# Kernel optimization log

Hardware: AMD Instinct MI355X
Metric: run time of the kernel (lower is better)

The kernel has to match this reference:

```python
import jax, jax.numpy as jnp
import numpy as np

N = 100000      # nodes
E = 1600000     # edges
D = 128         # hidden_dim
H = 8           # num_heads
DH = D // H     # per-head dim (out_dim in MultiHeadAttentionLayer)
EPS = 1e-5


def layer_norm(x, g, b):
    mu = jnp.mean(x, axis=-1, keepdims=True)
    var = jnp.var(x, axis=-1, keepdims=True)
    return (x - mu) * jax.lax.rsqrt(var + EPS) * g + b


def setup_inputs() -> dict:
    key = jax.random.key(0)
    ks = jax.random.split(key, 16)
    s = 1.0 / np.sqrt(D)
    inp = {
        "h": jax.random.normal(ks[0], (N, D), jnp.float32),
        "src": jax.random.randint(ks[1], (E,), 0, N, jnp.int32),
        "dst": jax.random.randint(ks[2], (E,), 0, N, jnp.int32),
        # attention projections (use_bias=False)
        "Wq": jax.random.uniform(ks[3], (D, D), jnp.float32, -s, s),
        "Wk": jax.random.uniform(ks[4], (D, D), jnp.float32, -s, s),
        "Wv": jax.random.uniform(ks[5], (D, D), jnp.float32, -s, s),
        # output projection O (bias=True)
        "Wo": jax.random.uniform(ks[6], (D, D), jnp.float32, -s, s),
        "bo": jnp.zeros((D,), jnp.float32),
        # layer norms
        "g1": jnp.ones((D,), jnp.float32),
        "b1": jnp.zeros((D,), jnp.float32),
        "g2": jnp.ones((D,), jnp.float32),
        "b2": jnp.zeros((D,), jnp.float32),
        # FFN
        "W1": jax.random.uniform(ks[7], (D, 2 * D), jnp.float32, -s, s),
        "c1": jnp.zeros((2 * D,), jnp.float32),
        "W2": jax.random.uniform(ks[8], (2 * D, D), jnp.float32, -1.0 / np.sqrt(2 * D), 1.0 / np.sqrt(2 * D)),
        "c2": jnp.zeros((D,), jnp.float32),
    }
    return inp


def reference(h, src, dst, Wq, Wk, Wv, Wo, bo, g1, b1, g2, b2, W1, c1, W2, c2):
    n = h.shape[0]
    Q = (h @ Wq).reshape(n, H, DH)
    K = (h @ Wk).reshape(n, H, DH)
    V = (h @ Wv).reshape(n, H, DH)

    # per-edge score: (K[src] * Q[dst]).sum(-1), scaled exp with clamp
    score = jnp.einsum('ehd,ehd->eh', K[src], Q[dst])          # [E, H]
    score = jnp.exp(jnp.clip(score / np.sqrt(DH), -5.0, 5.0))  # [E, H]

    # scatter-sum aggregation into destination nodes
    wV = jax.ops.segment_sum(V[src] * score[:, :, None], dst, num_segments=n)  # [N, H, DH]
    z = jax.ops.segment_sum(score, dst, num_segments=n)                        # [N, H]

    # possible_empty=True: divide only where z > 0
    zb = z[:, :, None]
    head_out = jnp.where(zb > 0, wV / jnp.where(zb > 0, zb, 1.0), wV)

    a = head_out.reshape(n, D) @ Wo + bo
    hh = layer_norm(h + a, g1, b1)
    ff = jax.nn.relu(hh @ W1 + c1) @ W2 + c2
    return layer_norm(hh + ff, g2, b2)
```

## Files before the change

### kernel.cpp

```cpp
#include <hip/hip_runtime.h>
#include <hip/hip_bf16.h>

#define D 128

typedef __attribute__((ext_vector_type(8))) short short8;
typedef __attribute__((ext_vector_type(4))) float float4v;
typedef __attribute__((ext_vector_type(2))) float float2v;

__device__ __forceinline__ float4v mfma16(short8 a, short8 b, float4v c) {
  return __builtin_amdgcn_mfma_f32_16x16x32_bf16(a, b, c, 0, 0, 0);
}
__device__ __forceinline__ float b2f(__hip_bfloat16 x) { return __bfloat162float(x); }
__device__ __forceinline__ __hip_bfloat16 f2b(float x) { return __float2bfloat16(x); }
__device__ __forceinline__ unsigned short f2b_bits(float x) {
  __hip_bfloat16 h = __float2bfloat16(x);
  return *reinterpret_cast<unsigned short*>(&h);
}

__device__ __forceinline__ float ldf(const float* p, size_t i) { return p[i]; }
__device__ __forceinline__ float ldf(const __hip_bfloat16* p, size_t i) { return b2f(p[i]); }
__device__ __forceinline__ void stf(float* p, size_t i, float v) { p[i] = v; }
__device__ __forceinline__ void stf(__hip_bfloat16* p, size_t i, float v) { p[i] = f2b(v); }

__device__ __forceinline__ void bar_lds() {
  asm volatile("s_waitcnt lgkmcnt(0)\n\ts_barrier" ::: "memory");
}

__device__ __forceinline__ float2v up2(unsigned w) {
  float2v r;
  r.x = __uint_as_float(w << 16);
  r.y = __uint_as_float(w & 0xffff0000u);
  return r;
}
__device__ __forceinline__ unsigned char f2fp8(float x) {
  int r = __builtin_amdgcn_cvt_pk_fp8_f32(x, x, 0, false);
  return (unsigned char)(r & 0xff);
}
__device__ __forceinline__ float2v cvt2lo(unsigned w) {
  return __builtin_amdgcn_cvt_pk_f32_fp8(w, false);
}
__device__ __forceinline__ float2v cvt2hi(unsigned w) {
  return __builtin_amdgcn_cvt_pk_f32_fp8(w, true);
}

__device__ __forceinline__ short8 cvt8(float4 u0, float4 u1) {
  short8 a;
  a[0] = (short)f2b_bits(u0.x); a[1] = (short)f2b_bits(u0.y);
  a[2] = (short)f2b_bits(u0.z); a[3] = (short)f2b_bits(u0.w);
  a[4] = (short)f2b_bits(u1.x); a[5] = (short)f2b_bits(u1.y);
  a[6] = (short)f2b_bits(u1.z); a[7] = (short)f2b_bits(u1.w);
  return a;
}

__global__ void k_cast_w(const float* __restrict__ wq, const float* __restrict__ wk,
                         const float* __restrict__ wv, const float* __restrict__ wo,
                         const float* __restrict__ w1, const float* __restrict__ w2,
                         __hip_bfloat16* __restrict__ oq, __hip_bfloat16* __restrict__ ok,
                         __hip_bfloat16* __restrict__ ov, __hip_bfloat16* __restrict__ oo,
                         __hip_bfloat16* __restrict__ o1, __hip_bfloat16* __restrict__ o2) {
  int i = blockIdx.x * 256 + threadIdx.x;
  if (i < 65536) {
    int m = i & 16383;
    int which = i >> 14;
    const float* s = (which == 0) ? wq : (which == 1) ? wk : (which == 2) ? wv : wo;
    __hip_bfloat16* o = (which == 0) ? oq : (which == 1) ? ok : (which == 2) ? ov : oo;
    int j = m & 7, t2 = m >> 3;
    int col = t2 & 127, cq = t2 >> 7;
    o[m] = f2b(s[((cq >> 2) * 32 + (cq & 3) * 8 + j) * 128 + col]);
  } else if (i < 98304) {
    int m = i - 65536;
    int j = m & 7, t2 = m >> 3;
    int col = t2 & 255, cq = t2 >> 8;
    o1[m] = f2b(w1[((cq >> 2) * 32 + (cq & 3) * 8 + j) * 256 + col]);
  } else {
    int m = i - 98304;
    int j = m & 7, t2 = m >> 3;
    int col = t2 & 127, cq = t2 >> 7;
    o2[m] = f2b(w2[((cq >> 2) * 32 + (cq & 3) * 8 + j) * 128 + col]);
  }
}

#define MAXB 512

__global__ void k_bhist(const int* __restrict__ dst, int* __restrict__ bh, int E) {
  __shared__ int cnt[MAXB];
  for (int i = threadIdx.x; i < MAXB; i += 256) cnt[i] = 0;
  __syncthreads();
  for (int e = blockIdx.x * 256 + threadIdx.x; e < E; e += gridDim.x * 256)
    atomicAdd(&cnt[dst[e] >> 8], 1);
  __syncthreads();
  for (int i = threadIdx.x; i < MAXB; i += 256)
    if (cnt[i]) atomicAdd(&bh[i], cnt[i]);
}

__global__ void k_bscan(const int* __restrict__ bh, int* __restrict__ bbase,
                        int* __restrict__ bcur, int B) {
  __shared__ int sd[MAXB];
  int t = threadIdx.x;
  int v = (t < B) ? bh[t] : 0;
  sd[t] = v;
  __syncthreads();
  for (int o = 1; o < MAXB; o <<= 1) {
    int x = (t >= o) ? sd[t - o] : 0;
    __syncthreads();
    sd[t] += x;
    __syncthreads();
  }
  if (t < B) {
    int e = sd[t] - v;
    bbase[t] = e;
    bcur[t] = e;
  }
}

__global__ __launch_bounds__(256) void k_bin(const int* __restrict__ src,
                                             const int* __restrict__ dst,
                                             int* __restrict__ bcur,
                                             uint2* __restrict__ binned, int E) {
  __shared__ int cnt[MAXB];
  __shared__ int base[MAXB];
  const int t = threadIdx.x;
  const int e0 = blockIdx.x * 4096;
  for (int i = t; i < MAXB; i += 256) cnt[i] = 0;
  __syncthreads();
  int myb[16], myr[16], ms[16], md[16];
#pragma unroll
  for (int j = 0; j < 16; ++j) {
    int e = e0 + j * 256 + t;
    if (e < E) {
      int d = dst[e];
      ms[j] = src[e];
      md[j] = d;
      int b = d >> 8;
      myb[j] = b;
      myr[j] = atomicAdd(&cnt[b], 1);
    } else {
      myb[j] = -1;
    }
  }
  __syncthreads();
  for (int i = t; i < MAXB; i += 256)
    base[i] = cnt[i] ? atomicAdd(&bcur[i], cnt[i]) : 0;
  __syncthreads();
#pragma unroll
  for (int j = 0; j < 16; ++j)
    if (myb[j] >= 0)
      binned[(size_t)base[myb[j]] + myr[j]] = make_uint2((unsigned)ms[j], (unsigned)md[j]);
}

__global__ __launch_bounds__(256) void k_fine(const uint2* __restrict__ binned,
                                              const int* __restrict__ bh,
                                              const int* __restrict__ bbase,
                                              int* __restrict__ deg,
                                              int* __restrict__ offs,
                                              int* __restrict__ csr, int N) {
  __shared__ int cnt[256];
  __shared__ int cur[256];
  __shared__ int sd[256];
  const int b = blockIdx.x, t = threadIdx.x;
  const int node0 = b << 8;
  cnt[t] = 0;
  __syncthreads();
  const int s0 = bbase[b], len = bh[b];
  for (int i = t; i < len; i += 256) atomicAdd(&cnt[binned[(size_t)s0 + i].y & 255], 1);
  __syncthreads();
  int v = cnt[t];
  sd[t] = v;
  __syncthreads();
  for (int o = 1; o < 256; o <<= 1) {
    int x = (t >= o) ? sd[t - o] : 0;
    __syncthreads();
    sd[t] += x;
    __syncthreads();
  }
  int excl = sd[t] - v;
  cur[t] = excl;
  int node = node0 + t;
  if (node < N) {
    deg[node] = v;
    offs[node] = s0 + excl;
  }
  __syncthreads();
  for (int i = t; i < len; i += 256) {
    uint2 ed = binned[(size_t)s0 + i];
    int p = atomicAdd(&cur[ed.y & 255], 1);
    csr[s0 + p] = (int)ed.x;
  }
}

__global__ __launch_bounds__(512) void gemm_qkv4(const float* __restrict__ A,
                                                 const short8* __restrict__ BqF,
                                                 const short8* __restrict__ BkF,
                                                 const short8* __restrict__ BvF,
                                                 __hip_bfloat16* __restrict__ Q,
                                                 unsigned char* __restrict__ KV8,
                                                 int Nrow) {
  const int t = threadIdx.x;
  const int lane = t & 63;
  const int ct = t >> 6;
  const int n = lane & 15, quad = lane >> 4;
  const short8* bq = BqF;
  const short8* bk = BkF;
  const short8* bv = BvF;
  const int fbase = quad * 128 + ct * 16 + n;
  const int ntiles = Nrow >> 4;
  const int koff = ct * 32 + ((n >> 3) << 4) + (n & 7);
  for (int rt = blockIdx.x; rt < ntiles; rt += gridDim.x) {
    asm volatile("" : "+v"(bq), "+v"(bk), "+v"(bv));
    const float* Ap = A + (size_t)(rt * 16 + n) * 128 + quad * 8;
    short8 a[4], fq[4], fk[4], fv[4];
#pragma unroll
    for (int c = 0; c < 4; ++c) {
      a[c] = cvt8(*(const float4*)(Ap + c * 32), *(const float4*)(Ap + c * 32 + 4));
      fq[c] = bq[fbase + c * 512];
      fk[c] = bk[fbase + c * 512];
      fv[c] = bv[fbase + c * 512];
    }
    float4v aq = {0.f, 0.f, 0.f, 0.f}, ak = aq, av = aq;
#pragma unroll
    for (int c = 0; c < 4; ++c) {
      aq = mfma16(a[c], fq[c], aq);
      ak = mfma16(a[c], fk[c], ak);
      av = mfma16(a[c], fv[c], av);
    }
#pragma unroll
    for (int r = 0; r < 4; ++r) {
      int grow = rt * 16 + quad * 4 + r;
      Q[(size_t)grow * 128 + ct * 16 + n] = f2b(aq[r]);
      size_t b = (size_t)grow * 256 + koff;
      KV8[b] = f2fp8(ak[r]);
      KV8[b + 8] = f2fp8(av[r]);
    }
  }
}

template <int K, typename TR, typename TO>
__global__ __launch_bounds__(512) void ln_gemm(const short* __restrict__ A,
                                               const short8* __restrict__ BF,
                                               const float* __restrict__ bias,
                                               const TR* __restrict__ resid,
                                               const float* __restrict__ gam,
                                               const float* __restrict__ bet,
                                               TO* __restrict__ Out, int Nrow) {
  __shared__ float tile[2][16][132];
  const int t = threadIdx.x;
  const int lane = t & 63;
  const int ct = t >> 6;
  const int n = lane & 15, quad = lane >> 4;
  const short8* bp = BF;
  const int fbase = quad * 128 + ct * 16 + n;
  float biasv = bias[ct * 16 + n];
  const int row2 = t >> 5, sub = t & 31;
  float ga0 = gam[sub],      ga1 = gam[sub + 32];
  float ga2 = gam[sub + 64], ga3 = gam[sub + 96];
  float be0 = bet[sub],      be1 = bet[sub + 32];
  float be2 = bet[sub + 64], be3 = bet[sub + 96];
  const int ntiles = Nrow >> 4;
  int pp = 0;
  for (int rt = blockIdx.x; rt < ntiles; rt += gridDim.x, pp ^= 1) {
    asm volatile("" : "+v"(bp));
    const short8* Ap = (const short8*)(A + (size_t)(rt * 16 + n) * K + quad * 8);
    short8 a[K / 32], bf[K / 32];
    float rs[4];
#pragma unroll
    for (int c = 0; c < K / 32; ++c) {
      a[c] = Ap[c * 4];
      bf[c] = bp[fbase + c * 512];
    }
#pragma unroll
    for (int r = 0; r < 4; ++r)
      rs[r] = ldf(resid, (size_t)(rt * 16 + quad * 4 + r) * 128 + ct * 16 + n);
    float4v acc = {0.f, 0.f, 0.f, 0.f};
#pragma unroll
    for (int c = 0; c < K / 32; ++c) acc = mfma16(a[c], bf[c], acc);
#pragma unroll
    for (int r = 0; r < 4; ++r)
      tile[pp][quad * 4 + r][ct * 16 + n] = acc[r] + biasv + rs[r];
    bar_lds();
    float x0 = tile[pp][row2][sub], x1 = tile[pp][row2][sub + 32];
    float x2 = tile[pp][row2][sub + 64], x3 = tile[pp][row2][sub + 96];
    float s = x0 + x1 + x2 + x3;
    float s2 = x0 * x0 + x1 * x1 + x2 * x2 + x3 * x3;
#pragma unroll
    for (int o = 16; o >= 1; o >>= 1) {
      s += __shfl_xor(s, o);
      s2 += __shfl_xor(s2, o);
    }
    float mean = s * 0.0078125f;
    float var = s2 * 0.0078125f - mean * mean;
    float rstd = rsqrtf(var + 1e-5f);
    size_t base = (size_t)(rt * 16 + row2) * 128;
    stf(Out, base + sub,      (x0 - mean) * rstd * ga0 + be0);
    stf(Out, base + sub + 32, (x1 - mean) * rstd * ga1 + be1);
    stf(Out, base + sub + 64, (x2 - mean) * rstd * ga2 + be2);
    stf(Out, base + sub + 96, (x3 - mean) * rstd * ga3 + be3);
  }
}

__global__ __launch_bounds__(512) void ffn_ln(const short* __restrict__ hh,
                                              const short8* __restrict__ W1F,
                                              const float* __restrict__ c1,
                                              const short8* __restrict__ W2F,
                                              const float* __restrict__ c2,
                                              const float* __restrict__ gam,
                                              const float* __restrict__ bet,
                                              float* __restrict__ Out, int Nrow) {
  __shared__ short mid[16][264];
  __shared__ float tile[16][132];
  const int t = threadIdx.x;
  const int lane = t & 63;
  const int wv = t >> 6;
  const int n = lane & 15, quad = lane >> 4;
  const short8* p1 = W1F;
  const short8* p2 = W2F;
  float b1v0 = c1[(wv * 2) * 16 + n], b1v1 = c1[(wv * 2 + 1) * 16 + n];
  float b2v = c2[wv * 16 + n];
  const int row2 = t >> 5, sub = t & 31;
  float ga0 = gam[sub],      ga1 = gam[sub + 32];
  float ga2 = gam[sub + 64], ga3 = gam[sub + 96];
  float be0 = bet[sub],      be1 = bet[sub + 32];
  float be2 = bet[sub + 64], be3 = bet[sub + 96];
  const int ntiles = Nrow >> 4;
  const __hip_bfloat16* hb = (const __hip_bfloat16*)hh;
  const int f1b0 = quad * 256 + (wv * 2) * 16 + n;
  const int f1b1 = quad * 256 + (wv * 2 + 1) * 16 + n;
  const int f2b = quad * 128 + wv * 16 + n;
  for (int rt = blockIdx.x; rt < ntiles; rt += gridDim.x) {
    asm volatile("" : "+v"(p1), "+v"(p2));
    const short8* Ap = (const short8*)(hh + (size_t)(rt * 16 + n) * 128 + quad * 8);
    short8 a[4], f1a[4], f1c[4], f2f[8];
    __hip_bfloat16 rs[4];
#pragma unroll
    for (int c = 0; c < 4; ++c) {
      a[c] = Ap[c * 4];
      f1a[c] = p1[f1b0 + c * 1024];
      f1c[c] = p1[f1b1 + c * 1024];
    }
#pragma unroll
    for (int c = 0; c < 8; ++c) f2f[c] = p2[f2b + c * 512];
#pragma unroll
    for (int r = 0; r < 4; ++r)
      rs[r] = hb[(size_t)(rt * 16 + quad * 4 + r) * 128 + wv * 16 + n];
    float4v a10 = {0.f, 0.f, 0.f, 0.f}, a11 = a10;
#pragma unroll
    for (int c = 0; c < 4; ++c) {
      a10 = mfma16(a[c], f1a[c], a10);
      a11 = mfma16(a[c], f1c[c], a11);
    }
#pragma unroll
    for (int r = 0; r < 4; ++r) {
      mid[quad * 4 + r][(wv * 2) * 16 + n] = (short)f2b_bits(fmaxf(a10[r] + b1v0, 0.f));
      mid[quad * 4 + r][(wv * 2 + 1) * 16 + n] = (short)f2b_bits(fmaxf(a11[r] + b1v1, 0.f));
    }
    bar_lds();
    float4v acc = {0.f, 0.f, 0.f, 0.f};
#pragma unroll
    for (int c = 0; c < 8; ++c) {
      short8 am = *(const short8*)&mid[n][quad * 8 + c * 32];
      acc = mfma16(am, f2f[c], acc);
    }
#pragma unroll
    for (int r = 0; r < 4; ++r)
      tile[quad * 4 + r][wv * 16 + n] = acc[r] + b2v + b2f(rs[r]);
    bar_lds();
    float x0 = tile[row2][sub], x1 = tile[row2][sub + 32];
    float x2 = tile[row2][sub + 64], x3 = tile[row2][sub + 96];
    float s = x0 + x1 + x2 + x3;
    float s2 = x0 * x0 + x1 * x1 + x2 * x2 + x3 * x3;
#pragma unroll
    for (int o = 16; o >= 1; o >>= 1) {
      s += __shfl_xor(s, o);
      s2 += __shfl_xor(s2, o);
    }
    float mean = s * 0.0078125f;
    float var = s2 * 0.0078125f - mean * mean;
    float rstd = rsqrtf(var + 1e-5f);
    size_t base = (size_t)(rt * 16 + row2) * 128;
    Out[base + sub]      = (x0 - mean) * rstd * ga0 + be0;
    Out[base + sub + 32] = (x1 - mean) * rstd * ga1 + be1;
    Out[base + sub + 64] = (x2 - mean) * rstd * ga2 + be2;
    Out[base + sub + 96] = (x3 - mean) * rstd * ga3 + be3;
    bar_lds();
  }
}

__global__ __launch_bounds__(256) void attn_agg5(const uint4* __restrict__ Q4,
                                                 const uint4* __restrict__ KV8,
                                                 const int* __restrict__ offs,
                                                 const int* __restrict__ deg,
                                                 const int* __restrict__ csr,
                                                 uint4* __restrict__ AT4, int N) {
  const int lane = threadIdx.x & 63;
  const int wv = threadIdx.x >> 6;
  const int e4 = lane >> 4;
  const int hd = (lane >> 1) & 7;
  const int hf = lane & 1;
  const int kvo = hd * 2 + hf;
  for (int node = blockIdx.x * 4 + wv; node < N; node += gridDim.x * 4) {
    uint4 qa = Q4[(size_t)node * 16 + kvo];
    float2v qv[4];
    qv[0] = up2(qa.x); qv[1] = up2(qa.y); qv[2] = up2(qa.z); qv[3] = up2(qa.w);
    float2v acc[4];
#pragma unroll
    for (int d = 0; d < 4; ++d) acc[d] = (float2v){0.f, 0.f};
    float z = 0.f;
    const int st = offs[node], dg = deg[node];
    if (dg > 0) {
      const int dgm1 = dg - 1;
      int s_cur = csr[st + min(e4, dgm1)];
      int s_nxt = (dg > 4) ? csr[st + min(4 + e4, dgm1)] : s_cur;
      uint4 ckv = KV8[(size_t)s_cur * 16 + kvo];
      int i = 0;
      while (true) {
        const bool more = (i + 4) < dg;
        uint4 nkv;
        int s_fut = s_nxt;
        if (more) {
          nkv = KV8[(size_t)s_nxt * 16 + kvo];
          s_fut = csr[st + min(i + 8 + e4, dgm1)];
        }
        float2v p2 = cvt2lo(ckv.x) * qv[0];
        p2 += cvt2hi(ckv.x) * qv[1];
        p2 += cvt2lo(ckv.y) * qv[2];
        p2 += cvt2hi(ckv.y) * qv[3];
        float p = p2.x + p2.y;
        p += __shfl_xor(p, 1);
        float sc = __expf(fminf(fmaxf(p * 0.25f, -5.f), 5.f));
        sc = ((i + e4) < dg) ? sc : 0.f;
        z += sc;
        float2v sv = {sc, sc};
        acc[0] += cvt2lo(ckv.z) * sv;
        acc[1] += cvt2hi(ckv.z) * sv;
        acc[2] += cvt2lo(ckv.w) * sv;
        acc[3] += cvt2hi(ckv.w) * sv;
        if (!more) break;
        ckv = nkv;
        s_nxt = s_fut;
        i += 4;
      }
    }
#pragma unroll
    for (int m = 16; m <= 32; m <<= 1) {
      z += __shfl_xor(z, m);
#pragma unroll
      for (int d = 0; d < 4; ++d) {
        acc[d].x += __shfl_xor(acc[d].x, m);
        acc[d].y += __shfl_xor(acc[d].y, m);
      }
    }
    if (e4 == 0) {
      float inv = (z > 0.f) ? 1.f / z : 1.f;
      unsigned r[4];
#pragma unroll
      for (int j = 0; j < 4; ++j)
        r[j] = (unsigned)f2b_bits(acc[j].x * inv) |
               ((unsigned)f2b_bits(acc[j].y * inv) << 16);
      AT4[(size_t)node * 16 + kvo] = make_uint4(r[0], r[1], r[2], r[3]);
    }
  }
}

extern "C" void kernel_launch(void* const* d_in, const int* in_sizes, int n_in,
                              void* d_out, int out_size, void* d_ws, size_t ws_size,
                              hipStream_t stream) {
  const float* h = (const float*)d_in[0];
  const int* src = (const int*)d_in[1];
  const int* dst = (const int*)d_in[2];
  const float* Wq = (const float*)d_in[3];
  const float* Wk = (const float*)d_in[4];
  const float* Wv = (const float*)d_in[5];
  const float* Wo = (const float*)d_in[6];
  const float* bo = (const float*)d_in[7];
  const float* g1 = (const float*)d_in[8];
  const float* b1 = (const float*)d_in[9];
  const float* g2 = (const float*)d_in[10];
  const float* b2 = (const float*)d_in[11];
  const float* W1 = (const float*)d_in[12];
  const float* c1 = (const float*)d_in[13];
  const float* W2 = (const float*)d_in[14];
  const float* c2 = (const float*)d_in[15];

  const int N = in_sizes[0] / D;
  const int E = in_sizes[1];
  const int B = (N + 255) >> 8;

  char* p = (char*)d_ws;
  auto carve = [&](size_t bytes) {
    char* r = p;
    p += (bytes + 255) & ~(size_t)255;
    return r;
  };
  short* ATb = (short*)carve((size_t)N * D * 2);
  short* Qb = (short*)carve((size_t)N * D * 2);
  unsigned char* KVb = (unsigned char*)carve((size_t)N * 256);
  short* wq = (short*)carve(16384 * 2);
  short* wk = (short*)carve(16384 * 2);
  short* wv = (short*)carve(16384 * 2);
  short* wo = (short*)carve(16384 * 2);
  short* w1 = (short*)carve(32768 * 2);
  short* w2 = (short*)carve(32768 * 2);
  int* deg = (int*)carve((size_t)N * 4);
  int* offs = (int*)carve((size_t)N * 4);
  int* bh = (int*)carve(MAXB * 4);
  int* bbase = (int*)carve(MAXB * 4);
  int* bcur = (int*)carve(MAXB * 4);
  uint2* binned = (uint2*)carve((size_t)E * 8);
  int* csr = (int*)carve((size_t)E * 4);
  short* hh = Qb;

  hipMemsetAsync(bh, 0, MAXB * 4, stream);
  k_bhist<<<1024, 256, 0, stream>>>(dst, bh, E);
  k_bscan<<<1, MAXB, 0, stream>>>(bh, bbase, bcur, B);
  k_bin<<<(E + 4095) / 4096, 256, 0, stream>>>(src, dst, bcur, binned, E);
  k_fine<<<B, 256, 0, stream>>>(binned, bh, bbase, deg, offs, csr, N);

  k_cast_w<<<512, 256, 0, stream>>>(Wq, Wk, Wv, Wo, W1, W2,
                                    (__hip_bfloat16*)wq, (__hip_bfloat16*)wk,
                                    (__hip_bfloat16*)wv, (__hip_bfloat16*)wo,
                                    (__hip_bfloat16*)w1, (__hip_bfloat16*)w2);

  gemm_qkv4<<<1536, 512, 0, stream>>>(h, (const short8*)wq, (const short8*)wk,
                                      (const short8*)wv, (__hip_bfloat16*)Qb, KVb, N);

  attn_agg5<<<(N + 3) >> 2, 256, 0, stream>>>((const uint4*)Qb, (const uint4*)KVb,
                                              offs, deg, csr, (uint4*)ATb, N);

  ln_gemm<128, float, __hip_bfloat16><<<1536, 512, 0, stream>>>(
      ATb, (const short8*)wo, bo, h, g1, b1, (__hip_bfloat16*)hh, N);
  ffn_ln<<<1536, 512, 0, stream>>>(hh, (const short8*)w1, c1, (const short8*)w2, c2,
                                   g2, b2, (float*)d_out, N);
}
```

Measured before the change: 427.1 us.

## Stage GEMM weights in LDS and prefetch next row tile in persistent kernels

Result: faster. 398.1 us (-6.8%).

```diff
diff --git a/kernel.cpp b/kernel.cpp
--- a/kernel.cpp
+++ b/kernel.cpp
@@ -188,40 +188,66 @@
   }
 }
 
-__global__ __launch_bounds__(512) void gemm_qkv4(const float* __restrict__ A,
-                                                 const short8* __restrict__ BqF,
-                                                 const short8* __restrict__ BkF,
-                                                 const short8* __restrict__ BvF,
+__global__ __launch_bounds__(512) void gemm_qkv5(const float* __restrict__ A,
+                                                 const uint4* __restrict__ wqF,
+                                                 const uint4* __restrict__ wkF,
+                                                 const uint4* __restrict__ wvF,
                                                  __hip_bfloat16* __restrict__ Q,
                                                  unsigned char* __restrict__ KV8,
                                                  int Nrow) {
+  __shared__ short W[3 * 16384];
   const int t = threadIdx.x;
+  {
+    uint4* W4 = (uint4*)W;
+    for (int i = t; i < 2048; i += 512) {
+      W4[i] = wqF[i];
+      W4[i + 2048] = wkF[i];
+      W4[i + 4096] = wvF[i];
+    }
+  }
+  __syncthreads();
   const int lane = t & 63;
   const int ct = t >> 6;
   const int n = lane & 15, quad = lane >> 4;
-  const short8* bq = BqF;
-  const short8* bk = BkF;
-  const short8* bv = BvF;
   const int fbase = quad * 128 + ct * 16 + n;
   const int ntiles = Nrow >> 4;
   const int koff = ct * 32 + ((n >> 3) << 4) + (n & 7);
-  for (int rt = blockIdx.x; rt < ntiles; rt += gridDim.x) {
-    asm volatile("" : "+v"(bq), "+v"(bk), "+v"(bv));
+  int rt = blockIdx.x;
+  if (rt >= ntiles) return;
+  float4 u[8];
+  {
     const float* Ap = A + (size_t)(rt * 16 + n) * 128 + quad * 8;
-    short8 a[4], fq[4], fk[4], fv[4];
 #pragma unroll
     for (int c = 0; c < 4; ++c) {
-      a[c] = cvt8(*(const float4*)(Ap + c * 32), *(const float4*)(Ap + c * 32 + 4));
-      fq[c] = bq[fbase + c * 512];
-      fk[c] = bk[fbase + c * 512];
-      fv[c] = bv[fbase + c * 512];
-    }
+      u[2 * c] = *(const float4*)(Ap + c * 32);
+      u[2 * c + 1] = *(const float4*)(Ap + c * 32 + 4);
+    }
+  }
+  while (true) {
+    const int rtn = rt + gridDim.x;
+    const bool more = rtn < ntiles;
+    float4 un[8];
+    if (more) {
+      const float* Ap = A + (size_t)(rtn * 16 + n) * 128 + quad * 8;
+#pragma unroll
+      for (int c = 0; c < 4; ++c) {
+        un[2 * c] = *(const float4*)(Ap + c * 32);
+        un[2 * c + 1] = *(const float4*)(Ap + c * 32 + 4);
+      }
+    }
+    short8 a[4];
+#pragma unroll
+    for (int c = 0; c < 4; ++c) a[c] = cvt8(u[2 * c], u[2 * c + 1]);
     float4v aq = {0.f, 0.f, 0.f, 0.f}, ak = aq, av = aq;
 #pragma unroll
     for (int c = 0; c < 4; ++c) {
-      aq = mfma16(a[c], fq[c], aq);
-      ak = mfma16(a[c], fk[c], ak);
-      av = mfma16(a[c], fv[c], av);
+      const int fo = (fbase + c * 512) * 8;
+      short8 fq = *(const short8*)&W[fo];
+      short8 fk = *(const short8*)&W[16384 + fo];
+      short8 fv = *(const short8*)&W[32768 + fo];
+      aq = mfma16(a[c], fq, aq);
+      ak = mfma16(a[c], fk, ak);
+      av = mfma16(a[c], fv, av);
     }
 #pragma unroll
     for (int r = 0; r < 4; ++r) {
@@ -231,23 +257,32 @@
       KV8[b] = f2fp8(ak[r]);
       KV8[b + 8] = f2fp8(av[r]);
     }
+    if (!more) break;
+#pragma unroll
+    for (int i = 0; i < 8; ++i) u[i] = un[i];
+    rt = rtn;
   }
 }
 
 template <int K, typename TR, typename TO>
 __global__ __launch_bounds__(512) void ln_gemm(const short* __restrict__ A,
-                                               const short8* __restrict__ BF,
+                                               const uint4* __restrict__ BF4,
                                                const float* __restrict__ bias,
                                                const TR* __restrict__ resid,
                                                const float* __restrict__ gam,
                                                const float* __restrict__ bet,
                                                TO* __restrict__ Out, int Nrow) {
-  __shared__ float tile[2][16][132];
+  __shared__ short W[K * 128];
+  __shared__ float tile[16][132];
   const int t = threadIdx.x;
+  {
+    uint4* W4 = (uint4*)W;
+    for (int i = t; i < K * 16; i += 512) W4[i] = BF4[i];
+  }
+  __syncthreads();
   const int lane = t & 63;
   const int ct = t >> 6;
   const int n = lane & 15, quad = lane >> 4;
-  const short8* bp = BF;
   const int fbase = quad * 128 + ct * 16 + n;
   float biasv = bias[ct * 16 + n];
   const int row2 = t >> 5, sub = t & 31;
@@ -256,29 +291,27 @@
   float be0 = bet[sub],      be1 = bet[sub + 32];
   float be2 = bet[sub + 64], be3 = bet[sub + 96];
   const int ntiles = Nrow >> 4;
-  int pp = 0;
-  for (int rt = blockIdx.x; rt < ntiles; rt += gridDim.x, pp ^= 1) {
-    asm volatile("" : "+v"(bp));
+  for (int rt = blockIdx.x; rt < ntiles; rt += gridDim.x) {
     const short8* Ap = (const short8*)(A + (size_t)(rt * 16 + n) * K + quad * 8);
-    short8 a[K / 32], bf[K / 32];
+    short8 a[K / 32];
     float rs[4];
 #pragma unroll
-    for (int c = 0; c < K / 32; ++c) {
-      a[c] = Ap[c * 4];
-      bf[c] = bp[fbase + c * 512];
-    }
+    for (int c = 0; c < K / 32; ++c) a[c] = Ap[c * 4];
 #pragma unroll
     for (int r = 0; r < 4; ++r)
       rs[r] = ldf(resid, (size_t)(rt * 16 + quad * 4 + r) * 128 + ct * 16 + n);
     float4v acc = {0.f, 0.f, 0.f, 0.f};
 #pragma unroll
-    for (int c = 0; c < K / 32; ++c) acc = mfma16(a[c], bf[c], acc);
+    for (int c = 0; c < K / 32; ++c) {
+      short8 bf = *(const short8*)&W[(fbase + c * 512) * 8];
+      acc = mfma16(a[c], bf, acc);
+    }
 #pragma unroll
     for (int r = 0; r < 4; ++r)
-      tile[pp][quad * 4 + r][ct * 16 + n] = acc[r] + biasv + rs[r];
+      tile[quad * 4 + r][ct * 16 + n] = acc[r] + biasv + rs[r];
     bar_lds();
-    float x0 = tile[pp][row2][sub], x1 = tile[pp][row2][sub + 32];
-    float x2 = tile[pp][row2][sub + 64], x3 = tile[pp][row2][sub + 96];
+    float x0 = tile[row2][sub], x1 = tile[row2][sub + 32];
+    float x2 = tile[row2][sub + 64], x3 = tile[row2][sub + 96];
     float s = x0 + x1 + x2 + x3;
     float s2 = x0 * x0 + x1 * x1 + x2 * x2 + x3 * x3;
 #pragma unroll
@@ -294,25 +327,35 @@
     stf(Out, base + sub + 32, (x1 - mean) * rstd * ga1 + be1);
     stf(Out, base + sub + 64, (x2 - mean) * rstd * ga2 + be2);
     stf(Out, base + sub + 96, (x3 - mean) * rstd * ga3 + be3);
+    bar_lds();
   }
 }
 
 __global__ __launch_bounds__(512) void ffn_ln(const short* __restrict__ hh,
-                                              const short8* __restrict__ W1F,
+                                              const uint4* __restrict__ W1F4,
                                               const float* __restrict__ c1,
-                                              const short8* __restrict__ W2F,
+                                              const uint4* __restrict__ W2F4,
                                               const float* __restrict__ c2,
                                               const float* __restrict__ gam,
                                               const float* __restrict__ bet,
                                               float* __restrict__ Out, int Nrow) {
+  __shared__ short W1[32768];
+  __shared__ short W2[32768];
   __shared__ short mid[16][264];
   __shared__ float tile[16][132];
   const int t = threadIdx.x;
+  {
+    uint4* a4 = (uint4*)W1;
+    uint4* b4 = (uint4*)W2;
+    for (int i = t; i < 4096; i += 512) {
+      a4[i] = W1F4[i];
+      b4[i] = W2F4[i];
+    }
+  }
+  __syncthreads();
   const int lane = t & 63;
   const int wv = t >> 6;
   const int n = lane & 15, quad = lane >> 4;
-  const short8* p1 = W1F;
-  const short8* p2 = W2F;
   float b1v0 = c1[(wv * 2) * 16 + n], b1v1 = c1[(wv * 2 + 1) * 16 + n];
   float b2v = c2[wv * 16 + n];
   const int row2 = t >> 5, sub = t & 31;
@@ -325,27 +368,38 @@
   const int f1b0 = quad * 256 + (wv * 2) * 16 + n;
   const int f1b1 = quad * 256 + (wv * 2 + 1) * 16 + n;
   const int f2b = quad * 128 + wv * 16 + n;
-  for (int rt = blockIdx.x; rt < ntiles; rt += gridDim.x) {
-    asm volatile("" : "+v"(p1), "+v"(p2));
+  int rt = blockIdx.x;
+  if (rt >= ntiles) return;
+  short8 a[4];
+  __hip_bfloat16 rs[4];
+  {
     const short8* Ap = (const short8*)(hh + (size_t)(rt * 16 + n) * 128 + quad * 8);
-    short8 a[4], f1a[4], f1c[4], f2f[8];
-    __hip_bfloat16 rs[4];
-#pragma unroll
-    for (int c = 0; c < 4; ++c) {
-      a[c] = Ap[c * 4];
-      f1a[c] = p1[f1b0 + c * 1024];
-      f1c[c] = p1[f1b1 + c * 1024];
-    }
-#pragma unroll
-    for (int c = 0; c < 8; ++c) f2f[c] = p2[f2b + c * 512];
+#pragma unroll
+    for (int c = 0; c < 4; ++c) a[c] = Ap[c * 4];
 #pragma unroll
     for (int r = 0; r < 4; ++r)
       rs[r] = hb[(size_t)(rt * 16 + quad * 4 + r) * 128 + wv * 16 + n];
+  }
+  while (true) {
+    const int rtn = rt + gridDim.x;
+    const bool more = rtn < ntiles;
+    short8 an[4];
+    __hip_bfloat16 rsn[4];
+    if (more) {
+      const short8* Ap = (const short8*)(hh + (size_t)(rtn * 16 + n) * 128 + quad * 8);
+#pragma unroll
+      for (int c = 0; c < 4; ++c) an[c] = Ap[c * 4];
+#pragma unroll
+      for (int r = 0; r < 4; ++r)
+        rsn[r] = hb[(size_t)(rtn * 16 + quad * 4 + r) * 128 + wv * 16 + n];
+    }
     float4v a10 = {0.f, 0.f, 0.f, 0.f}, a11 = a10;
 #pragma unroll
     for (int c = 0; c < 4; ++c) {
-      a10 = mfma16(a[c], f1a[c], a10);
-      a11 = mfma16(a[c], f1c[c], a11);
+      short8 f1a = *(const short8*)&W1[(f1b0 + c * 1024) * 8];
+      short8 f1c = *(const short8*)&W1[(f1b1 + c * 1024) * 8];
+      a10 = mfma16(a[c], f1a, a10);
+      a11 = mfma16(a[c], f1c, a11);
     }
 #pragma unroll
     for (int r = 0; r < 4; ++r) {
@@ -357,7 +411,8 @@
 #pragma unroll
     for (int c = 0; c < 8; ++c) {
       short8 am = *(const short8*)&mid[n][quad * 8 + c * 32];
-      acc = mfma16(am, f2f[c], acc);
+      short8 f2 = *(const short8*)&W2[(f2b + c * 512) * 8];
+      acc = mfma16(am, f2, acc);
     }
 #pragma unroll
     for (int r = 0; r < 4; ++r)
@@ -381,6 +436,12 @@
     Out[base + sub + 64] = (x2 - mean) * rstd * ga2 + be2;
     Out[base + sub + 96] = (x3 - mean) * rstd * ga3 + be3;
     bar_lds();
+    if (!more) break;
+#pragma unroll
+    for (int c = 0; c < 4; ++c) a[c] = an[c];
+#pragma unroll
+    for (int r = 0; r < 4; ++r) rs[r] = rsn[r];
+    rt = rtn;
   }
 }
 
@@ -519,14 +580,14 @@
                                     (__hip_bfloat16*)wv, (__hip_bfloat16*)wo,
                                     (__hip_bfloat16*)w1, (__hip_bfloat16*)w2);
 
-  gemm_qkv4<<<1536, 512, 0, stream>>>(h, (const short8*)wq, (const short8*)wk,
-                                      (const short8*)wv, (__hip_bfloat16*)Qb, KVb, N);
+  gemm_qkv5<<<256, 512, 0, stream>>>(h, (const uint4*)wq, (const uint4*)wk,
+                                     (const uint4*)wv, (__hip_bfloat16*)Qb, KVb, N);
 
   attn_agg5<<<(N + 3) >> 2, 256, 0, stream>>>((const uint4*)Qb, (const uint4*)KVb,
                                               offs, deg, csr, (uint4*)ATb, N);
 
-  ln_gemm<128, float, __hip_bfloat16><<<1536, 512, 0, stream>>>(
-      ATb, (const short8*)wo, bo, h, g1, b1, (__hip_bfloat16*)hh, N);
-  ffn_ln<<<1536, 512, 0, stream>>>(hh, (const short8*)w1, c1, (const short8*)w2, c2,
-                                   g2, b2, (float*)d_out, N);
-}
+  ln_gemm<128, float, __hip_bfloat16><<<768, 512, 0, stream>>>(
+      ATb, (const uint4*)wo, bo, h, g1, b1, (__hip_bfloat16*)hh, N);
+  ffn_ln<<<256, 512, 0, stream>>>(hh, (const uint4*)w1, c1, (const uint4*)w2, c2,
+                                  g2, b2, (float*)d_out, N);
+}
```
